# Optimization experiments

Measured on AMD Instinct MI355X. Metric: run time of the kernel, lower is better.

Reference implementation:

```python
import jax, jax.numpy as jnp
import numpy as np

N, E, C, H, DH, NB, NA, FC = 30000, 480000, 128, 8, 16, 32, 16, 64
AH = H * DH  # 128 = attn-heads feature dim = mul_alpha


def smooth_leaky_relu(x, alpha=0.2):
    # Equiformer SmoothLeakyReLU: (1+a)/2 * x + (1-a)/2 * x * (2*sigmoid(x) - 1)
    return 0.5 * (1.0 + alpha) * x + 0.5 * (1.0 - alpha) * x * (2.0 * jax.nn.sigmoid(x) - 1.0)


def setup_inputs() -> dict:
    key = jax.random.key(0)
    ks = jax.random.split(key, 20)

    def rn(k, shape, scale=1.0):
        return jax.random.normal(k, shape, dtype=jnp.float32) * scale

    inp = {
        "node_feats": rn(ks[0], (N, C)),
        "node_attr": rn(ks[1], (N, NA)),
        "edge_attr": rn(ks[2], (E, 1)),          # scalar spherical-harmonic channel
        "edge_embedding": rn(ks[3], (E, NB)),     # radial basis embedding
        # message_src_proj (bias) / message_dst_proj (no bias)
        "W_src": rn(ks[4], (C, C), 1.0 / np.sqrt(C)),
        "b_src": jnp.zeros((C,), jnp.float32),
        "W_dst": rn(ks[5], (C, C), 1.0 / np.sqrt(C)),
        # radial network (dtp_rad) for external TP weights
        "W_fc1": rn(ks[6], (NB + 2 * NA, FC), 1.0 / np.sqrt(NB + 2 * NA)),
        "b_fc1": jnp.zeros((FC,), jnp.float32),
        "W_fc2": rn(ks[7], (FC, FC), 1.0 / np.sqrt(FC)),
        "b_fc2": jnp.zeros((FC,), jnp.float32),
        "W_fc3": rn(ks[8], (FC, C), 1.0 / np.sqrt(FC)),
        # attention_score_net
        "W_alpha": rn(ks[9], (C, AH), 1.0 / np.sqrt(C)),
        # edge_message_net.lin (followed by gate)
        "W_lin": rn(ks[10], (C, C), 1.0 / np.sqrt(C)),
        # value_net internal depthwise-TP weights + its linear
        "w_int": rn(ks[11], (C,)),
        "W_val": rn(ks[12], (C, AH), 1.0 / np.sqrt(C)),
        # attention_dot [num_heads, mul_alpha_head]
        "att_dot": rn(ks[13], (H, DH), 1.0 / np.sqrt(DH)),
        # output projection
        "W_out": rn(ks[14], (AH, C), 1.0 / np.sqrt(AH)),
        "b_out": jnp.zeros((C,), jnp.float32),
        "edge_src": jax.random.randint(ks[15], (E,), 0, N),
        "edge_dst": jax.random.randint(ks[16], (E,), 0, N),
    }
    return inp


def reference(node_feats, node_attr, edge_attr, edge_embedding,
              W_src, b_src, W_dst,
              W_fc1, b_fc1, W_fc2, b_fc2, W_fc3,
              W_alpha, W_lin, w_int, W_val, att_dot, W_out, b_out,
              edge_src, edge_dst):
    # node projections then gather to edges
    msg_src = node_feats @ W_src + b_src
    msg_dst = node_feats @ W_dst
    message = msg_src[edge_src] + msg_dst[edge_dst]                    # [E, C]

    # radial net on concat(edge_embedding, src_attr, dst_attr)
    wf = jnp.concatenate([edge_embedding, node_attr[edge_src], node_attr[edge_dst]], axis=-1)
    h = jax.nn.silu(wf @ W_fc1 + b_fc1)
    h = jax.nn.silu(h @ W_fc2 + b_fc2)
    weight = h @ W_fc3                                                 # [E, C] depthwise-TP weights

    # depthwise tensor product with scalar edge_attr, radial-weighted
    message = message * edge_attr * weight                             # [E, C]

    # attention scores -> heads
    scores = (message @ W_alpha).reshape(E, H, DH)                     # [E, H, DH]

    # value path: lin + gate (SiLU on scalars), internal-weight dtp, lin -> heads
    value = jax.nn.silu(message @ W_lin)                               # [E, C]
    value = value * edge_attr * w_int                                  # [E, C]
    value = (value @ W_val).reshape(E, H, DH)                          # [E, H, DH]

    scores = smooth_leaky_relu(scores)
    logits = jnp.einsum('ehk,hk->eh', scores, att_dot)                 # [E, H]

    # segment softmax over destination nodes (torch_geometric.utils.softmax)
    m = jax.ops.segment_max(logits, edge_dst, num_segments=N)          # [N, H]
    m = jnp.where(jnp.isfinite(m), m, 0.0)
    ex = jnp.exp(logits - m[edge_dst])
    den = jax.ops.segment_sum(ex, edge_dst, num_segments=N)
    alpha = ex / (den[edge_dst] + 1e-16)                               # [E, H]

    # attention-weighted scatter-add aggregation
    out = jax.ops.segment_sum(value * alpha[:, :, None], edge_dst, num_segments=N)  # [N, H, DH]
    out = out.reshape(N, AH)
    return out @ W_out + b_out                                         # [N, C]
```

## Files before the change

kernel.cpp:

```cpp
#include <hip/hip_runtime.h>
#include <hip/hip_bf16.h>
#include <cstdint>
#include <cstddef>


typedef unsigned short u16;
typedef unsigned int u32;
typedef __attribute__((ext_vector_type(8))) short bf16x8;
typedef __attribute__((ext_vector_type(4))) float f32x4;

union fu_ { float f; u32 u; };
static __device__ __forceinline__ float lo2f(u32 v) { fu_ x; x.u = v << 16; return x.f; }
static __device__ __forceinline__ float hi2f(u32 v) { fu_ x; x.u = v & 0xFFFF0000u; return x.f; }
static __device__ __forceinline__ u16 f2bf(float f) {
    union { __hip_bfloat16 h; u16 u; } c;
    c.h = __float2bfloat16(f);
    return c.u;
}
static __device__ __forceinline__ u32 pack2(float a, float b) {
    return (u32)f2bf(a) | ((u32)f2bf(b) << 16);
}
static __device__ __forceinline__ float sigmoidf_(float x) { return 1.0f / (1.0f + __expf(-x)); }
static __device__ __forceinline__ float siluf_(float x)    { return x * sigmoidf_(x); }
static __device__ __forceinline__ float slreluf_(float x)  { return x * (0.2f + 0.8f * sigmoidf_(x)); }

#define MFMA16(a, b, c) __builtin_amdgcn_mfma_f32_16x16x32_bf16((a), (b), (c), 0, 0, 0)

static __device__ __forceinline__ bf16x8 ld8f_bf(const float* __restrict__ p) {
    const float4 x = *reinterpret_cast<const float4*>(p);
    const float4 y = *reinterpret_cast<const float4*>(p + 4);
    bf16x8 r;
    r[0] = (short)f2bf(x.x); r[1] = (short)f2bf(x.y);
    r[2] = (short)f2bf(x.z); r[3] = (short)f2bf(x.w);
    r[4] = (short)f2bf(y.x); r[5] = (short)f2bf(y.y);
    r[6] = (short)f2bf(y.z); r[7] = (short)f2bf(y.w);
    return r;
}

__global__ void hist_k(const int* __restrict__ dst, int* __restrict__ deg, int E) {
    int i = blockIdx.x * blockDim.x + threadIdx.x;
    if (i < E) atomicAdd(&deg[dst[i]], 1);
}

__global__ void scan_k(const int* __restrict__ deg, int* __restrict__ rowptr,
                       int* __restrict__ cursor, int n) {
    __shared__ int part[1024];
    const int t = threadIdx.x;
    const int C = (n + 1023) / 1024;
    const int lo = t * C;
    const int hi = (lo + C < n) ? (lo + C) : n;
    int s = 0;
    for (int i = lo; i < hi; ++i) s += deg[i];
    part[t] = s;
    __syncthreads();
    for (int off = 1; off < 1024; off <<= 1) {
        int v = part[t];
        int u = (t >= off) ? part[t - off] : 0;
        __syncthreads();
        part[t] = v + u;
        __syncthreads();
    }
    int excl = (t == 0) ? 0 : part[t - 1];
    for (int i = lo; i < hi; ++i) {
        rowptr[i] = excl;
        cursor[i] = excl;
        excl += deg[i];
    }
    if (t == 1023) rowptr[n] = part[1023];
}

__global__ void fill_k(const int* __restrict__ dst, int* __restrict__ cursor,
                       int* __restrict__ eids, int E) {
    int i = blockIdx.x * blockDim.x + threadIdx.x;
    if (i < E) {
        int d = dst[i];
        int p = atomicAdd(&cursor[d], 1);
        eids[p] = i;
    }
}

__global__ void prep_w_k(const float* __restrict__ Wa, const float* __restrict__ Wl,
                         const float* __restrict__ Wv,
                         const float* __restrict__ W1, const float* __restrict__ W2,
                         const float* __restrict__ W3,
                         const float* __restrict__ Wsrc, const float* __restrict__ Wdst,
                         const float* __restrict__ Wout,
                         u16* __restrict__ Wct, u16* __restrict__ Wvt,
                         u16* __restrict__ Bt1, u16* __restrict__ Bt2,
                         u16* __restrict__ Bt3,
                         u16* __restrict__ Wst, u16* __restrict__ Wdt,
                         u16* __restrict__ Wot) {
    int idx = blockIdx.x * 256 + threadIdx.x;
    if (idx < 32768) {
        int c = idx >> 7, k = idx & 127;
        float v = (c < 128) ? Wa[(size_t)k * 128 + c] : Wl[(size_t)k * 128 + (c - 128)];
        Wct[idx] = f2bf(v);
    } else if (idx < 49152) {
        int t = idx - 32768;
        int j = t >> 7, c = t & 127;
        Wvt[t] = f2bf(Wv[(size_t)c * 128 + j]);
    } else if (idx < 53248) {
        int t = idx - 49152;
        int c = t >> 6, k = t & 63;
        Bt1[t] = f2bf(W1[(size_t)k * 64 + c]);
    } else if (idx < 57344) {
        int t = idx - 53248;
        int c = t >> 6, k = t & 63;
        Bt2[t] = f2bf(W2[(size_t)k * 64 + c]);
    } else if (idx < 65536) {
        int t = idx - 57344;
        int c = t >> 6, k = t & 63;
        Bt3[t] = f2bf(W3[(size_t)k * 128 + c]);
    } else if (idx < 81920) {
        int t = idx - 65536;
        int c = t >> 7, k = t & 127;
        Wst[t] = f2bf(Wsrc[(size_t)k * 128 + c]);
    } else if (idx < 98304) {
        int t = idx - 81920;
        int c = t >> 7, k = t & 127;
        Wdt[t] = f2bf(Wdst[(size_t)k * 128 + c]);
    } else if (idx < 114688) {
        int t = idx - 98304;
        int c = t >> 7, k = t & 127;
        Wot[t] = f2bf(Wout[(size_t)k * 128 + c]);
    }
}

__global__ __launch_bounds__(256) void proj_mfma_k(const float* __restrict__ A,
                                                   const u16* __restrict__ Wt,
                                                   const float* __restrict__ bias,
                                                   float* __restrict__ Out, int M) {
    const int tid  = threadIdx.x;
    const int lane = tid & 63;
    const int w    = tid >> 6;
    const int lr   = lane & 15;
    const int lg   = lane >> 4;
    const int e0   = blockIdx.x * 64;

    f32x4 acc[4][2];
#pragma unroll
    for (int m = 0; m < 4; ++m)
#pragma unroll
        for (int n = 0; n < 2; ++n) acc[m][n] = (f32x4)(0.0f);

#pragma unroll
    for (int ks = 0; ks < 4; ++ks) {
        const int kk = lg * 8 + ks * 32;
        bf16x8 a[4], b[2];
#pragma unroll
        for (int m = 0; m < 4; ++m) {
            int row = e0 + lr + 16 * m;
            row = (row < M) ? row : (M - 1);
            a[m] = ld8f_bf(&A[(size_t)row * 128 + kk]);
        }
#pragma unroll
        for (int n = 0; n < 2; ++n) {
            const int c = 32 * w + 16 * n + lr;
            b[n] = *reinterpret_cast<const bf16x8*>(&Wt[(size_t)c * 128 + kk]);
        }
#pragma unroll
        for (int m = 0; m < 4; ++m)
#pragma unroll
            for (int n = 0; n < 2; ++n) acc[m][n] = MFMA16(a[m], b[n], acc[m][n]);
    }

#pragma unroll
    for (int n = 0; n < 2; ++n) {
        const int j = 32 * w + 16 * n + lr;
        const float bv = bias ? bias[j] : 0.0f;
#pragma unroll
        for (int m = 0; m < 4; ++m)
#pragma unroll
            for (int i = 0; i < 4; ++i) {
                const int row = e0 + 16 * m + 4 * lg + i;
                if (row < M) Out[(size_t)row * 128 + j] = acc[m][n][i] + bv;
            }
    }
}

__global__ __launch_bounds__(256, 3) void msg_attn_k(
    const float* __restrict__ eemb, const float* __restrict__ nattr,
    const float* __restrict__ ea,
    const int* __restrict__ src, const int* __restrict__ dst,
    const int* __restrict__ eids,
    const u16* __restrict__ Bt1, const float* __restrict__ b1,
    const u16* __restrict__ Bt2, const float* __restrict__ b2,
    const u16* __restrict__ Bt3,
    const float* __restrict__ Ps, const float* __restrict__ Pd,
    const u16* __restrict__ Wct, const u16* __restrict__ Wvt,
    const float* __restrict__ att_dot, const float* __restrict__ w_int,
    float* __restrict__ LG, u16* __restrict__ V, int E) {
    __shared__ __align__(16) char smem[35840];
    char* regA   = smem;
    char* regB   = smem + 16384;
    float* lgs   = (float*)(smem + 32768);
    int*   eid_l = (int*)(smem + 34816);
    int*   src_l = eid_l + 64;
    int*   dst_l = src_l + 64;
    float* ea_l  = (float*)(dst_l + 64);

    const int tid  = threadIdx.x;
    const int lane = tid & 63;
    const int w    = tid >> 6;
    const int lr   = lane & 15;
    const int lg   = lane >> 4;
    const int e0   = blockIdx.x * 64;

    if (tid < 64) {
        int slot = e0 + tid;
        int e = (slot < E) ? eids[slot] : eids[E - 1];
        eid_l[tid] = e;
        src_l[tid] = src[e];
        dst_l[tid] = dst[e];
        ea_l[tid]  = ea[e];
    }
    __syncthreads();

    {
        f32x4 acc1[4];
#pragma unroll
        for (int m = 0; m < 4; ++m) acc1[m] = (f32x4)(0.0f);
#pragma unroll
        for (int ks = 0; ks < 2; ++ks) {
            const int kk = lg * 8 + ks * 32;
            bf16x8 a[4];
#pragma unroll
            for (int m = 0; m < 4; ++m) {
                const int r = lr + 16 * m;
                const float* ap;
                if (kk < 32)      ap = &eemb[(size_t)eid_l[r] * 32 + kk];
                else if (kk < 48) ap = &nattr[(size_t)src_l[r] * 16 + (kk - 32)];
                else              ap = &nattr[(size_t)dst_l[r] * 16 + (kk - 48)];
                a[m] = ld8f_bf(ap);
            }
            const bf16x8 b = *reinterpret_cast<const bf16x8*>(&Bt1[(size_t)(16 * w + lr) * 64 + kk]);
#pragma unroll
            for (int m = 0; m < 4; ++m) acc1[m] = MFMA16(a[m], b, acc1[m]);
        }
        const int c = 16 * w + lr;
        const float bias = b1[c];
#pragma unroll
        for (int m = 0; m < 4; ++m)
#pragma unroll
            for (int i = 0; i < 4; ++i) {
                const int r = 16 * m + 4 * lg + i;
                const int byte = (r * 128 + c * 2) ^ ((r & 7) << 4);
                *reinterpret_cast<u16*>(regA + byte) = f2bf(siluf_(acc1[m][i] + bias));
            }
    }
    __syncthreads();

    {
        f32x4 acc2[4];
#pragma unroll
        for (int m = 0; m < 4; ++m) acc2[m] = (f32x4)(0.0f);
#pragma unroll
        for (int ks = 0; ks < 2; ++ks) {
            const int kk = lg * 8 + ks * 32;
            bf16x8 a[4];
#pragma unroll
            for (int m = 0; m < 4; ++m) {
                const int r = lr + 16 * m;
                const int byte = (r * 128 + kk * 2) ^ ((r & 7) << 4);
                a[m] = *reinterpret_cast<const bf16x8*>(regA + byte);
            }
            const bf16x8 b = *reinterpret_cast<const bf16x8*>(&Bt2[(size_t)(16 * w + lr) * 64 + kk]);
#pragma unroll
            for (int m = 0; m < 4; ++m) acc2[m] = MFMA16(a[m], b, acc2[m]);
        }
        const int c = 16 * w + lr;
        const float bias = b2[c];
#pragma unroll
        for (int m = 0; m < 4; ++m)
#pragma unroll
            for (int i = 0; i < 4; ++i) {
                const int r = 16 * m + 4 * lg + i;
                const int byte = (r * 128 + c * 2) ^ ((r & 7) << 4);
                *reinterpret_cast<u16*>(regA + 8192 + byte) = f2bf(siluf_(acc2[m][i] + bias));
            }
    }
    __syncthreads();

    {
        f32x4 acc3[2][4];
#pragma unroll
        for (int n = 0; n < 2; ++n)
#pragma unroll
            for (int m = 0; m < 4; ++m) acc3[n][m] = (f32x4)(0.0f);
#pragma unroll
        for (int ks = 0; ks < 2; ++ks) {
            const int kk = lg * 8 + ks * 32;
            bf16x8 a[4];
#pragma unroll
            for (int m = 0; m < 4; ++m) {
                const int r = lr + 16 * m;
                const int byte = (r * 128 + kk * 2) ^ ((r & 7) << 4);
                a[m] = *reinterpret_cast<const bf16x8*>(regA + 8192 + byte);
            }
            bf16x8 b[2];
#pragma unroll
            for (int n = 0; n < 2; ++n) {
                const int c = 32 * w + 16 * n + lr;
                b[n] = *reinterpret_cast<const bf16x8*>(&Bt3[(size_t)c * 64 + kk]);
            }
#pragma unroll
            for (int n = 0; n < 2; ++n)
#pragma unroll
                for (int m = 0; m < 4; ++m) acc3[n][m] = MFMA16(a[m], b[n], acc3[n][m]);
        }
#pragma unroll
        for (int n = 0; n < 2; ++n) {
            const int c = 32 * w + 16 * n + lr;
#pragma unroll
            for (int m = 0; m < 4; ++m)
#pragma unroll
                for (int i = 0; i < 4; ++i) {
                    const int r = 16 * m + 4 * lg + i;
                    const int byte = (r * 256 + c * 2) ^ ((r & 7) << 4);
                    *reinterpret_cast<u16*>(regB + byte) = f2bf(acc3[n][m][i]);
                }
        }
    }
    __syncthreads();

#pragma unroll
    for (int t = 0; t < 4; ++t) {
        const int idx = tid + 256 * t;
        const int r = idx >> 4;
        const int c8 = (idx & 15) * 8;
        if (e0 + r >= E) continue;
        const int byte = (r * 256 + c8 * 2) ^ ((r & 7) << 4);
        const uint4 wv = *reinterpret_cast<const uint4*>(regB + byte);
        const float wt[8] = {lo2f(wv.x), hi2f(wv.x), lo2f(wv.y), hi2f(wv.y),
                             lo2f(wv.z), hi2f(wv.z), lo2f(wv.w), hi2f(wv.w)};
        const int s = src_l[r], d = dst_l[r];
        const float eav = ea_l[r];
        const float4 ps0 = *reinterpret_cast<const float4*>(&Ps[(size_t)s * 128 + c8]);
        const float4 ps1 = *reinterpret_cast<const float4*>(&Ps[(size_t)s * 128 + c8 + 4]);
        const float4 pd0 = *reinterpret_cast<const float4*>(&Pd[(size_t)d * 128 + c8]);
        const float4 pd1 = *reinterpret_cast<const float4*>(&Pd[(size_t)d * 128 + c8 + 4]);
        float m[8];
        m[0] = (ps0.x + pd0.x) * eav * wt[0];
        m[1] = (ps0.y + pd0.y) * eav * wt[1];
        m[2] = (ps0.z + pd0.z) * eav * wt[2];
        m[3] = (ps0.w + pd0.w) * eav * wt[3];
        m[4] = (ps1.x + pd1.x) * eav * wt[4];
        m[5] = (ps1.y + pd1.y) * eav * wt[5];
        m[6] = (ps1.z + pd1.z) * eav * wt[6];
        m[7] = (ps1.w + pd1.w) * eav * wt[7];
        u32 p0 = pack2(m[0], m[1]), p1 = pack2(m[2], m[3]);
        u32 p2 = pack2(m[4], m[5]), p3 = pack2(m[6], m[7]);
        *reinterpret_cast<uint4*>(regB + byte) = make_uint4(p0, p1, p2, p3);
    }
    __syncthreads();

    const int c0w = w * 64;
#pragma unroll
    for (int n = 0; n < 4; ++n) {
        f32x4 accn[4];
#pragma unroll
        for (int m = 0; m < 4; ++m) accn[m] = (f32x4)(0.0f);
#pragma unroll
        for (int ks = 0; ks < 4; ++ks) {
            const int kk = lg * 8 + ks * 32;
            const bf16x8 b = *reinterpret_cast<const bf16x8*>(
                &Wct[(size_t)(c0w + 16 * n + lr) * 128 + kk]);
#pragma unroll
            for (int m = 0; m < 4; ++m) {
                const int r = lr + 16 * m;
                const int byte = (r * 256 + kk * 2) ^ ((r & 7) << 4);
                const bf16x8 am = *reinterpret_cast<const bf16x8*>(regB + byte);
                accn[m] = MFMA16(am, b, accn[m]);
            }
        }
        if (w < 2) {
            const float ad = att_dot[c0w + 16 * n + lr];
            const int h = 4 * w + n;
#pragma unroll
            for (int m = 0; m < 4; ++m) {
#pragma unroll
                for (int i = 0; i < 4; ++i) {
                    float s = slreluf_(accn[m][i]) * ad;
                    s += __shfl_xor(s, 1);
                    s += __shfl_xor(s, 2);
                    s += __shfl_xor(s, 4);
                    s += __shfl_xor(s, 8);
                    if (lr == 0) lgs[(16 * m + 4 * lg + i) * 8 + h] = s;
                }
            }
        } else {
            const int cc = 64 * (w - 2) + 16 * n + lr;
            const float wi = w_int[cc];
#pragma unroll
            for (int m = 0; m < 4; ++m) {
#pragma unroll
                for (int i = 0; i < 4; ++i) {
                    const int r = 16 * m + 4 * lg + i;
                    const float v1 = siluf_(accn[m][i]) * ea_l[r] * wi;
                    const int byte = (r * 256 + cc * 2) ^ ((r & 7) << 4);
                    *reinterpret_cast<u16*>(regA + byte) = f2bf(v1);
                }
            }
        }
    }
    __syncthreads();

    {
        f32x4 acc2[4][2];
#pragma unroll
        for (int m = 0; m < 4; ++m)
#pragma unroll
            for (int n = 0; n < 2; ++n) acc2[m][n] = (f32x4)(0.0f);
#pragma unroll
        for (int ks = 0; ks < 4; ++ks) {
            const int kk = lg * 8 + ks * 32;
            bf16x8 a2[4], b2[2];
#pragma unroll
            for (int m = 0; m < 4; ++m) {
                const int r = lr + 16 * m;
                const int byte = (r * 256 + kk * 2) ^ ((r & 7) << 4);
                a2[m] = *reinterpret_cast<const bf16x8*>(regA + byte);
            }
#pragma unroll
            for (int n = 0; n < 2; ++n) {
                const int j = 32 * w + 16 * n + lr;
                b2[n] = *reinterpret_cast<const bf16x8*>(&Wvt[(size_t)j * 128 + kk]);
            }
#pragma unroll
            for (int m = 0; m < 4; ++m)
#pragma unroll
                for (int n = 0; n < 2; ++n) acc2[m][n] = MFMA16(a2[m], b2[n], acc2[m][n]);
        }
        u16* Vout = (u16*)regB;
#pragma unroll
        for (int n = 0; n < 2; ++n) {
            const int j = 32 * w + 16 * n + lr;
#pragma unroll
            for (int m = 0; m < 4; ++m)
#pragma unroll
                for (int i = 0; i < 4; ++i) {
                    const int r = 16 * m + 4 * lg + i;
                    Vout[r * 128 + j] = f2bf(acc2[m][n][i]);
                }
        }
    }
    __syncthreads();

    const uint4* vo = reinterpret_cast<const uint4*>(regB);
#pragma unroll
    for (int t = 0; t < 4; ++t) {
        const int idx = tid + 256 * t;
        const int row = idx >> 4;
        if (e0 + row < E)
            *reinterpret_cast<uint4*>(&V[(size_t)e0 * 128 + idx * 8]) = vo[idx];
    }
    if (tid < 128) {
        const int row = tid >> 1;
        if (e0 + row < E)
            *reinterpret_cast<float4*>(&LG[(size_t)e0 * 8 + tid * 4]) =
                *reinterpret_cast<const float4*>(&lgs[tid * 4]);
    }
}

__global__ __launch_bounds__(256) void aggregate_k(const int* __restrict__ rowptr,
                                                   const float* __restrict__ LG,
                                                   const u16* __restrict__ V,
                                                   float* __restrict__ ACC, int Nn) {
    const int node = blockIdx.x * 4 + (threadIdx.x >> 6);
    const int lane = threadIdx.x & 63;
    if (node >= Nn) return;
    const int s = rowptr[node], t = rowptr[node + 1];
    const int h = lane >> 3;
    float a0 = 0.0f, a1 = 0.0f, ds = 0.0f;
    for (int i = s; i < t; ++i) {
        const float exv = __expf(LG[(size_t)i * 8 + h]);
        const u32 vv = *reinterpret_cast<const u32*>(&V[(size_t)i * 128 + lane * 2]);
        a0 += exv * lo2f(vv);
        a1 += exv * hi2f(vv);
        ds += exv;
    }
    const float inv = 1.0f / (ds + 1e-16f);
    ACC[(size_t)node * 128 + lane * 2]     = a0 * inv;
    ACC[(size_t)node * 128 + lane * 2 + 1] = a1 * inv;
}

extern "C" void kernel_launch(void* const* d_in, const int* in_sizes, int n_in,
                              void* d_out, int out_size, void* d_ws, size_t ws_size,
                              hipStream_t stream) {
    const float* node_feats = (const float*)d_in[0];
    const float* node_attr  = (const float*)d_in[1];
    const float* edge_attr  = (const float*)d_in[2];
    const float* edge_emb   = (const float*)d_in[3];
    const float* W_src      = (const float*)d_in[4];
    const float* b_src      = (const float*)d_in[5];
    const float* W_dst      = (const float*)d_in[6];
    const float* W_fc1      = (const float*)d_in[7];
    const float* b_fc1      = (const float*)d_in[8];
    const float* W_fc2      = (const float*)d_in[9];
    const float* b_fc2      = (const float*)d_in[10];
    const float* W_fc3      = (const float*)d_in[11];
    const float* W_alpha    = (const float*)d_in[12];
    const float* W_lin      = (const float*)d_in[13];
    const float* w_int      = (const float*)d_in[14];
    const float* W_val      = (const float*)d_in[15];
    const float* att_dot    = (const float*)d_in[16];
    const float* W_out      = (const float*)d_in[17];
    const float* b_out      = (const float*)d_in[18];
    const int* esrc         = (const int*)d_in[19];
    const int* edst         = (const int*)d_in[20];

    const int Nn = in_sizes[0] / 128;
    const int E  = in_sizes[19];

    char* w = (char*)d_ws;
    auto alloc = [&](size_t bytes) {
        char* p = w;
        w += (bytes + 255) & ~(size_t)255;
        return p;
    };
    u16* V      = (u16*)alloc((size_t)E * 128 * 2);
    float* LG   = (float*)alloc((size_t)E * 8 * 4);
    float* Psrc = (float*)alloc((size_t)Nn * 128 * 4);
    float* ACC  = Psrc;
    float* Pdst = (float*)alloc((size_t)Nn * 128 * 4);
    int* deg    = (int*)alloc((size_t)Nn * 4);
    int* rowptr = (int*)alloc((size_t)(Nn + 1) * 4);
    int* cursor = (int*)alloc((size_t)Nn * 4);
    int* eids   = (int*)alloc((size_t)E * 4);
    u16* Wct    = (u16*)alloc(32768 * 2);
    u16* Wvt    = (u16*)alloc(16384 * 2);
    u16* Bt1    = (u16*)alloc(4096 * 2);
    u16* Bt2    = (u16*)alloc(4096 * 2);
    u16* Bt3    = (u16*)alloc(8192 * 2);
    u16* Wst    = (u16*)alloc(16384 * 2);
    u16* Wdt    = (u16*)alloc(16384 * 2);
    u16* Wot    = (u16*)alloc(16384 * 2);

    hipMemsetAsync(deg, 0, (size_t)Nn * 4, stream);
    hist_k<<<(E + 255) / 256, 256, 0, stream>>>(edst, deg, E);
    scan_k<<<1, 1024, 0, stream>>>(deg, rowptr, cursor, Nn);
    fill_k<<<(E + 255) / 256, 256, 0, stream>>>(edst, cursor, eids, E);
    prep_w_k<<<448, 256, 0, stream>>>(W_alpha, W_lin, W_val, W_fc1, W_fc2, W_fc3,
                                      W_src, W_dst, W_out,
                                      Wct, Wvt, Bt1, Bt2, Bt3, Wst, Wdt, Wot);

    const int nb_node = (Nn + 63) / 64;
    const int nb_e    = (E + 63) / 64;

    proj_mfma_k<<<nb_node, 256, 0, stream>>>(node_feats, Wst, b_src, Psrc, Nn);
    proj_mfma_k<<<nb_node, 256, 0, stream>>>(node_feats, Wdt, nullptr, Pdst, Nn);

    msg_attn_k<<<nb_e, 256, 0, stream>>>(edge_emb, node_attr, edge_attr, esrc, edst, eids,
                                         Bt1, b_fc1, Bt2, b_fc2, Bt3,
                                         Psrc, Pdst, Wct, Wvt, att_dot, w_int,
                                         LG, V, E);

    aggregate_k<<<(Nn + 3) / 4, 256, 0, stream>>>(rowptr, LG, V, ACC, Nn);

    proj_mfma_k<<<nb_node, 256, 0, stream>>>(ACC, Wot, b_out, (float*)d_out, Nn);
}
```

Baseline: 499.2 us.

## Fuse aggregation with output projection and add XCD-aware block swizzle

```diff
diff --git a/kernel.cpp b/kernel.cpp
--- a/kernel.cpp
+++ b/kernel.cpp
@@ -35,6 +35,12 @@
     r[4] = (short)f2bf(y.x); r[5] = (short)f2bf(y.y);
     r[6] = (short)f2bf(y.z); r[7] = (short)f2bf(y.w);
     return r;
+}
+
+static __device__ __forceinline__ int xcd_swz(int orig, int nwg) {
+    const int q = nwg >> 3, rr = nwg & 7;
+    const int xcd = orig & 7, idx = orig >> 3;
+    return (xcd < rr ? xcd * (q + 1) : rr * (q + 1) + (xcd - rr) * q) + idx;
 }
 
 __global__ void hist_k(const int* __restrict__ dst, int* __restrict__ deg, int E) {
@@ -178,7 +184,7 @@
     }
 }
 
-__global__ __launch_bounds__(256, 3) void msg_attn_k(
+__global__ __launch_bounds__(256, 4) void msg_attn_k(
     const float* __restrict__ eemb, const float* __restrict__ nattr,
     const float* __restrict__ ea,
     const int* __restrict__ src, const int* __restrict__ dst,
@@ -204,7 +210,7 @@
     const int w    = tid >> 6;
     const int lr   = lane & 15;
     const int lg   = lane >> 4;
-    const int e0   = blockIdx.x * 64;
+    const int e0   = xcd_swz(blockIdx.x, gridDim.x) * 64;
 
     if (tid < 64) {
         int slot = e0 + tid;
@@ -462,26 +468,91 @@
     }
 }
 
-__global__ __launch_bounds__(256) void aggregate_k(const int* __restrict__ rowptr,
-                                                   const float* __restrict__ LG,
-                                                   const u16* __restrict__ V,
-                                                   float* __restrict__ ACC, int Nn) {
-    const int node = blockIdx.x * 4 + (threadIdx.x >> 6);
-    const int lane = threadIdx.x & 63;
-    if (node >= Nn) return;
-    const int s = rowptr[node], t = rowptr[node + 1];
+__global__ __launch_bounds__(256) void agg_out_k(const int* __restrict__ rowptr,
+                                                 const float* __restrict__ LG,
+                                                 const u16* __restrict__ V,
+                                                 const u16* __restrict__ Wot,
+                                                 const float* __restrict__ b_out,
+                                                 float* __restrict__ Out, int Nn) {
+    __shared__ __align__(16) char accs[64 * 256];
+
+    const int tid  = threadIdx.x;
+    const int lane = tid & 63;
+    const int w    = tid >> 6;
+    const int lr   = lane & 15;
+    const int lg   = lane >> 4;
+    const int n0   = xcd_swz(blockIdx.x, gridDim.x) * 64;
+
     const int h = lane >> 3;
-    float a0 = 0.0f, a1 = 0.0f, ds = 0.0f;
-    for (int i = s; i < t; ++i) {
-        const float exv = __expf(LG[(size_t)i * 8 + h]);
-        const u32 vv = *reinterpret_cast<const u32*>(&V[(size_t)i * 128 + lane * 2]);
-        a0 += exv * lo2f(vv);
-        a1 += exv * hi2f(vv);
-        ds += exv;
-    }
-    const float inv = 1.0f / (ds + 1e-16f);
-    ACC[(size_t)node * 128 + lane * 2]     = a0 * inv;
-    ACC[(size_t)node * 128 + lane * 2 + 1] = a1 * inv;
+    for (int t = 0; t < 16; ++t) {
+        const int node = n0 + 4 * t + w;
+        const int r = 4 * t + w;
+        if (node < Nn) {
+            const int s = rowptr[node], tt = rowptr[node + 1];
+            float a0 = 0.0f, a1 = 0.0f, ds = 0.0f;
+            int i = s;
+            for (; i + 1 < tt; i += 2) {
+                const float ex0 = __expf(LG[(size_t)i * 8 + h]);
+                const float ex1 = __expf(LG[(size_t)(i + 1) * 8 + h]);
+                const u32 v0 = *reinterpret_cast<const u32*>(&V[(size_t)i * 128 + lane * 2]);
+                const u32 v1 = *reinterpret_cast<const u32*>(&V[(size_t)(i + 1) * 128 + lane * 2]);
+                a0 += ex0 * lo2f(v0) + ex1 * lo2f(v1);
+                a1 += ex0 * hi2f(v0) + ex1 * hi2f(v1);
+                ds += ex0 + ex1;
+            }
+            if (i < tt) {
+                const float ex0 = __expf(LG[(size_t)i * 8 + h]);
+                const u32 v0 = *reinterpret_cast<const u32*>(&V[(size_t)i * 128 + lane * 2]);
+                a0 += ex0 * lo2f(v0);
+                a1 += ex0 * hi2f(v0);
+                ds += ex0;
+            }
+            const float inv = 1.0f / (ds + 1e-16f);
+            const int byte = (r * 256 + lane * 4) ^ ((r & 7) << 4);
+            *reinterpret_cast<u32*>(accs + byte) = pack2(a0 * inv, a1 * inv);
+        }
+    }
+    __syncthreads();
+
+    f32x4 acc[4][2];
+#pragma unroll
+    for (int m = 0; m < 4; ++m)
+#pragma unroll
+        for (int n = 0; n < 2; ++n) acc[m][n] = (f32x4)(0.0f);
+
+#pragma unroll
+    for (int ks = 0; ks < 4; ++ks) {
+        const int kk = lg * 8 + ks * 32;
+        bf16x8 a[4], b[2];
+#pragma unroll
+        for (int m = 0; m < 4; ++m) {
+            const int r = lr + 16 * m;
+            const int byte = (r * 256 + kk * 2) ^ ((r & 7) << 4);
+            a[m] = *reinterpret_cast<const bf16x8*>(accs + byte);
+        }
+#pragma unroll
+        for (int n = 0; n < 2; ++n) {
+            const int c = 32 * w + 16 * n + lr;
+            b[n] = *reinterpret_cast<const bf16x8*>(&Wot[(size_t)c * 128 + kk]);
+        }
+#pragma unroll
+        for (int m = 0; m < 4; ++m)
+#pragma unroll
+            for (int n = 0; n < 2; ++n) acc[m][n] = MFMA16(a[m], b[n], acc[m][n]);
+    }
+
+#pragma unroll
+    for (int n = 0; n < 2; ++n) {
+        const int j = 32 * w + 16 * n + lr;
+        const float bv = b_out[j];
+#pragma unroll
+        for (int m = 0; m < 4; ++m)
+#pragma unroll
+            for (int i = 0; i < 4; ++i) {
+                const int row = n0 + 16 * m + 4 * lg + i;
+                if (row < Nn) Out[(size_t)row * 128 + j] = acc[m][n][i] + bv;
+            }
+    }
 }
 
 extern "C" void kernel_launch(void* const* d_in, const int* in_sizes, int n_in,
@@ -521,7 +592,6 @@
     u16* V      = (u16*)alloc((size_t)E * 128 * 2);
     float* LG   = (float*)alloc((size_t)E * 8 * 4);
     float* Psrc = (float*)alloc((size_t)Nn * 128 * 4);
-    float* ACC  = Psrc;
     float* Pdst = (float*)alloc((size_t)Nn * 128 * 4);
     int* deg    = (int*)alloc((size_t)Nn * 4);
     int* rowptr = (int*)alloc((size_t)(Nn + 1) * 4);
@@ -555,7 +625,5 @@
                                          Psrc, Pdst, Wct, Wvt, att_dot, w_int,
                                          LG, V, E);
 
-    aggregate_k<<<(Nn + 3) / 4, 256, 0, stream>>>(rowptr, LG, V, ACC, Nn);
-
-    proj_mfma_k<<<nb_node, 256, 0, stream>>>(ACC, Wot, b_out, (float*)d_out, Nn);
-}
+    agg_out_k<<<nb_node, 256, 0, stream>>>(rowptr, LG, V, Wot, b_out, (float*)d_out, Nn);
+}
```

Measured after the change: 498.6 us. No clear change (-0.1%).
